# Performance work log

Hardware: AMD Instinct MI355X
Metric: run time of the kernel (lower is better)

## Reference

```python
import jax, jax.numpy as jnp
import numpy as np

B, N, CIN, COUT = 4, 4096, 64, 64

def setup_inputs() -> dict:
    key = jax.random.key(0)
    k1, k2, k3, k4, k5 = jax.random.split(key, 5)
    X = jax.random.normal(k1, (B, N, CIN), dtype=jnp.float32)
    A = jax.random.uniform(k2, (N, N), dtype=jnp.float32)
    weight1 = jax.random.normal(k3, (CIN, COUT), dtype=jnp.float32) * 0.05
    weight2 = jax.random.normal(k4, (1 * COUT, COUT), dtype=jnp.float32) * 0.05
    alpha = jax.random.normal(k5, (2 * COUT, 1), dtype=jnp.float32) * 0.05
    return {"X": X, "A": A, "weight1": weight1, "weight2": weight2, "alpha": alpha}

def reference(X, A, weight1, weight2, alpha):
    n = A.shape[0]
    c = weight1.shape[1]
    b = X.shape[0]
    # add self loops on the adjacency diagonal
    idx = jnp.arange(n)
    adj = A.at[idx, idx].set(1.0)
    # node transform: [B,N,C]
    out = jnp.matmul(X, weight1)
    # edge feature (P=1): [N,N,1], row-normalized over j (axis=1)
    E = adj[:, :, None]
    E_wave = E / E.sum(axis=1, keepdims=True)
    # attention scores via rank-1 decomposition of alpha
    att_l = jnp.matmul(out, alpha[:c])   # [B,N,1]
    att_r = jnp.matmul(out, alpha[c:])   # [B,N,1]
    scores = jax.nn.leaky_relu(att_l @ jnp.swapaxes(att_r, 1, 2))  # [B,N,N]
    # exp + edge-feature weighting: [P,B,N,N]
    att = jnp.einsum('bij,ijp->pbij', jnp.exp(scores), E_wave)
    # manual softmax-style normalization over neighbors j
    att = att / att.sum(axis=-1, keepdims=True)
    # aggregate: [B,N,P,C] -> [B,N,P*C]
    agg = jnp.einsum('pbij,bjc->bipc', att, out).reshape(b, n, -1)
    return jnp.matmul(agg, weight2)
```

## Files before the change

### kernel.cpp

```cpp
#include <hip/hip_runtime.h>
#include <hip/hip_bf16.h>

typedef __attribute__((ext_vector_type(8))) short short8;
typedef __attribute__((ext_vector_type(4))) float floatx4;
typedef unsigned int u32;

#define NN 4096

static __device__ __forceinline__ unsigned f2bf_rne(float x) {
    union { float f; unsigned u; } v; v.f = x;
    unsigned r = v.u + 0x7fffu + ((v.u >> 16) & 1u);
    return r >> 16;
}
static __device__ __forceinline__ float bf2f(unsigned hi) {
    union { unsigned u; float f; } v; v.u = hi << 16; return v.f;
}

__global__ __launch_bounds__(256, 4)
void prep_kernel(const float* __restrict__ X,
                 const float* __restrict__ W1,
                 const float* __restrict__ W2,
                 const float* __restrict__ alpha,
                 unsigned short* __restrict__ Gt,
                 float* __restrict__ lv,
                 float* __restrict__ rv) {
    __shared__ __align__(16) char sm[53248];
    float* W1s  = (float*)sm;
    float* W2s  = (float*)(sm + 17408);
    float* Wcst = (float*)(sm + 34816);
    float* w1s  = (float*)(sm + 52224);
    float* als  = (float*)(sm + 52736);
    float* GsT  = (float*)sm;

    const int t = threadIdx.x;
    const int row0 = blockIdx.x * 64;
    const int b = row0 >> 12, n0 = row0 & (NN - 1);
    const int w = t >> 6, lane = t & 63;
    const int m = lane & 15, q = lane >> 4;

    const int row = row0 + w * 16 + m;
    const float* xp = X + (size_t)row * 64;
    float4 x0 = *(const float4*)(xp + q * 8);
    float4 x1 = *(const float4*)(xp + q * 8 + 4);
    float4 x2 = *(const float4*)(xp + 32 + q * 8);
    float4 x3 = *(const float4*)(xp + 32 + q * 8 + 4);

    #pragma unroll
    for (int s = 0; s < 4; ++s) {
        int idx = s * 1024 + t * 4;
        int r = idx >> 6, cc = idx & 63;
        *(float4*)&W1s[r * 68 + cc] = *(const float4*)(W1 + idx);
        *(float4*)&W2s[r * 68 + cc] = *(const float4*)(W2 + idx);
    }
    if (t < 128) als[t] = alpha[t];
    __syncthreads();

    {
        const int k = t >> 2, nq = t & 3;
        float acc[16];
        #pragma unroll
        for (int i = 0; i < 16; ++i) acc[i] = 0.f;
        for (int mm = 0; mm < 64; ++mm) {
            float w1v = W1s[k * 68 + mm];
            #pragma unroll
            for (int i = 0; i < 16; ++i)
                acc[i] += w1v * W2s[mm * 68 + nq * 16 + i];
        }
        #pragma unroll
        for (int i = 0; i < 16; ++i)
            Wcst[(nq * 16 + i) * 68 + k] = acc[i];
    }
    if (t < 64) {
        float sl = 0.f, sr = 0.f;
        for (int cc2 = 0; cc2 < 64; ++cc2) {
            float wv = W1s[t * 68 + cc2];
            sl += wv * als[cc2];
            sr += wv * als[64 + cc2];
        }
        w1s[t] = sl; w1s[64 + t] = sr;
    }
    __syncthreads();

    const float xs[16] = {x0.x,x0.y,x0.z,x0.w, x1.x,x1.y,x1.z,x1.w,
                          x2.x,x2.y,x2.z,x2.w, x3.x,x3.y,x3.z,x3.w};

    float pl = 0.f, pr = 0.f;
    #pragma unroll
    for (int ks = 0; ks < 2; ++ks)
        #pragma unroll
        for (int j = 0; j < 8; ++j) {
            int k = ks * 32 + q * 8 + j;
            float xv = xs[ks * 8 + j];
            pl += xv * w1s[k];
            pr += xv * w1s[64 + k];
        }
    pl += __shfl_xor(pl, 16, 64); pl += __shfl_xor(pl, 32, 64);
    pr += __shfl_xor(pr, 16, 64); pr += __shfl_xor(pr, 32, 64);
    if (q == 0) { lv[row] = pl; rv[row] = pr; }

    short8 ah[2], al[2];
    #pragma unroll
    for (int ks = 0; ks < 2; ++ks)
        #pragma unroll
        for (int j = 0; j < 8; ++j) {
            float f = xs[ks * 8 + j];
            unsigned hb = f2bf_rne(f);
            float res = f - bf2f(hb);
            ah[ks][j] = (short)hb;
            al[ks][j] = (short)f2bf_rne(res);
        }

    short8 bfr[4][2];
    #pragma unroll
    for (int nt = 0; nt < 4; ++nt)
        #pragma unroll
        for (int ks = 0; ks < 2; ++ks) {
            const float* wp = &Wcst[(nt * 16 + m) * 68 + ks * 32 + q * 8];
            float4 w0 = *(const float4*)wp;
            float4 w1 = *(const float4*)(wp + 4);
            short8 bf;
            bf[0] = (short)f2bf_rne(w0.x); bf[1] = (short)f2bf_rne(w0.y);
            bf[2] = (short)f2bf_rne(w0.z); bf[3] = (short)f2bf_rne(w0.w);
            bf[4] = (short)f2bf_rne(w1.x); bf[5] = (short)f2bf_rne(w1.y);
            bf[6] = (short)f2bf_rne(w1.z); bf[7] = (short)f2bf_rne(w1.w);
            bfr[nt][ks] = bf;
        }

    floatx4 acc[4] = {{0,0,0,0},{0,0,0,0},{0,0,0,0},{0,0,0,0}};
    #pragma unroll
    for (int ks = 0; ks < 2; ++ks)
        #pragma unroll
        for (int nt = 0; nt < 4; ++nt) {
            acc[nt] = __builtin_amdgcn_mfma_f32_16x16x32_bf16(ah[ks], bfr[nt][ks], acc[nt], 0, 0, 0);
            acc[nt] = __builtin_amdgcn_mfma_f32_16x16x32_bf16(al[ks], bfr[nt][ks], acc[nt], 0, 0, 0);
        }

    __syncthreads();
    #pragma unroll
    for (int nt = 0; nt < 4; ++nt)
        #pragma unroll
        for (int rg = 0; rg < 4; ++rg)
            GsT[(nt * 16 + m) * 68 + w * 16 + q * 4 + rg] = acc[nt][rg];
    __syncthreads();
    unsigned* Gu = (unsigned*)Gt;
    #pragma unroll
    for (int it2 = 0; it2 < 8; ++it2) {
        int c2 = (t >> 5) + it2 * 8;
        int np = t & 31;
        unsigned lo = f2bf_rne(GsT[c2 * 68 + 2 * np]);
        unsigned hi = f2bf_rne(GsT[c2 * 68 + 2 * np + 1]);
        Gu[(((((size_t)(b * 64 + c2)) << 12) + n0) >> 1) + np] = lo | (hi << 16);
    }
}

__global__ __launch_bounds__(1024, 4)
void attn_kernel(const float* __restrict__ A,
                 const unsigned short* __restrict__ Gt,
                 const float* __restrict__ lv,
                 const float* __restrict__ rv,
                 float* __restrict__ out) {
    __shared__ __align__(16) char sm[61440];
    unsigned short* Gs = (unsigned short*)sm;

    const int bx = blockIdx.x;
    const int i0 = (bx & 63) * 64;
    const int b  = bx >> 6;
    const int t = threadIdx.x;
    const int wave = t >> 6, lane = t & 63;
    const int grp = wave >> 2, wsub = wave & 3;
    const int m = lane & 15, q = lane >> 4;
    const int irE = wsub * 16 + m;
    const int irS = wsub * 16 + (lane >> 2);
    const int jseg = lane & 3;

    const float* aRow = A + (size_t)(i0 + irE) * NN + grp * 1024 + q * 8;
    const float* rvp  = rv + (size_t)b * NN + grp * 1024 + q * 8;
    const unsigned short* gRow = Gt + (((size_t)(b * 64 + irS)) << 12) + grp * 1024 + jseg * 8;

    const float li = lv[b * NN + i0 + irE] * 1.44269504f;
    const float li001 = li * 0.01f;
    const bool diag_grp = ((i0 >> 10) == grp);
    const int jd = (i0 + irE) - grp * 1024;

    const int soff = irS * 40 + jseg * 8;
    unsigned short* GsG = Gs + grp * 2560;

    short8 sg = *(const short8*)(gRow);
    float4 a0E = *(const float4*)(aRow);
    float4 a1E = *(const float4*)(aRow + 4);
    float4 r0E = *(const float4*)(rvp);
    float4 r1E = *(const float4*)(rvp + 4);
    float4 a0O = *(const float4*)(aRow + 32);
    float4 a1O = *(const float4*)(aRow + 36);
    float4 r0O = *(const float4*)(rvp + 32);
    float4 r1O = *(const float4*)(rvp + 36);
    *(short8*)&GsG[soff] = sg;
    sg = *(const short8*)(gRow + 32);
    asm volatile("s_waitcnt lgkmcnt(0)" ::: "memory");
    __builtin_amdgcn_s_barrier();
    __builtin_amdgcn_sched_barrier(0);

    floatx4 acc0 = {0,0,0,0}, acc1 = {0,0,0,0}, acc2 = {0,0,0,0}, acc3 = {0,0,0,0};
    float dsum = 0.f;

    auto genE = [&](float4 a0, float4 a1, float4 r0, float4 r1, int chunk) -> short8 {
        float aa[8] = {a0.x, a0.y, a0.z, a0.w, a1.x, a1.y, a1.z, a1.w};
        if (diag_grp && ((jd >> 5) == chunk)) {
            const int dd = jd - (chunk * 32 + q * 8);
            #pragma unroll
            for (int e = 0; e < 8; ++e) if (dd == e) aa[e] = 1.0f;
        }
        const float rr[8] = {r0.x, r0.y, r0.z, r0.w, r1.x, r1.y, r1.z, r1.w};
        unsigned up[8];
        #pragma unroll
        for (int e = 0; e < 8; ++e) {
            float s = fmaxf(li * rr[e], li001 * rr[e]);
            float ev = __builtin_amdgcn_exp2f(s) * aa[e];
            unsigned u = __float_as_uint(ev) + 0x8000u;
            up[e] = u;
            dsum += __uint_as_float(u & 0xffff0000u);
        }
        union { unsigned u[4]; short8 s8; } cv;
        cv.u[0] = __builtin_amdgcn_perm(up[1], up[0], 0x07060302u);
        cv.u[1] = __builtin_amdgcn_perm(up[3], up[2], 0x07060302u);
        cv.u[2] = __builtin_amdgcn_perm(up[5], up[4], 0x07060302u);
        cv.u[3] = __builtin_amdgcn_perm(up[7], up[6], 0x07060302u);
        return cv.s8;
    };

    for (int cc = 0; cc < 32; cc += 2) {
        {
            *(short8*)&GsG[((cc + 1) % 3) * 10240 + soff] = sg;
            { const int jn = (cc + 2 < 32) ? (cc + 2) * 32 : 0;
              sg = *(const short8*)(gRow + jn); }
            const short8 afr = genE(a0E, a1E, r0E, r1E, cc);
            { const int jn = (cc + 2 < 32) ? (cc + 2) * 32 : 0;
              a0E = *(const float4*)(aRow + jn);
              a1E = *(const float4*)(aRow + jn + 4);
              r0E = *(const float4*)(rvp + jn);
              r1E = *(const float4*)(rvp + jn + 4); }
            const unsigned short* rb = &GsG[(cc % 3) * 10240];
            const short8 b0 = *(const short8*)&rb[( m) * 40 + q * 8];
            const short8 b1 = *(const short8*)&rb[(16 + m) * 40 + q * 8];
            const short8 b2 = *(const short8*)&rb[(32 + m) * 40 + q * 8];
            const short8 b3 = *(const short8*)&rb[(48 + m) * 40 + q * 8];
            acc0 = __builtin_amdgcn_mfma_f32_16x16x32_bf16(afr, b0, acc0, 0, 0, 0);
            acc1 = __builtin_amdgcn_mfma_f32_16x16x32_bf16(afr, b1, acc1, 0, 0, 0);
            acc2 = __builtin_amdgcn_mfma_f32_16x16x32_bf16(afr, b2, acc2, 0, 0, 0);
            acc3 = __builtin_amdgcn_mfma_f32_16x16x32_bf16(afr, b3, acc3, 0, 0, 0);
            asm volatile("s_waitcnt lgkmcnt(0)" ::: "memory");
            __builtin_amdgcn_s_barrier();
            __builtin_amdgcn_sched_barrier(0);
        }
        {
            *(short8*)&GsG[((cc + 2) % 3) * 10240 + soff] = sg;
            { const int jn = (cc + 3 < 32) ? (cc + 3) * 32 : 0;
              sg = *(const short8*)(gRow + jn); }
            const short8 afr = genE(a0O, a1O, r0O, r1O, cc + 1);
            { const int jn = (cc + 3 < 32) ? (cc + 3) * 32 : 0;
              a0O = *(const float4*)(aRow + jn);
              a1O = *(const float4*)(aRow + jn + 4);
              r0O = *(const float4*)(rvp + jn);
              r1O = *(const float4*)(rvp + jn + 4); }
            const unsigned short* rb = &GsG[((cc + 1) % 3) * 10240];
            const short8 b0 = *(const short8*)&rb[( m) * 40 + q * 8];
            const short8 b1 = *(const short8*)&rb[(16 + m) * 40 + q * 8];
            const short8 b2 = *(const short8*)&rb[(32 + m) * 40 + q * 8];
            const short8 b3 = *(const short8*)&rb[(48 + m) * 40 + q * 8];
            acc0 = __builtin_amdgcn_mfma_f32_16x16x32_bf16(afr, b0, acc0, 0, 0, 0);
            acc1 = __builtin_amdgcn_mfma_f32_16x16x32_bf16(afr, b1, acc1, 0, 0, 0);
            acc2 = __builtin_amdgcn_mfma_f32_16x16x32_bf16(afr, b2, acc2, 0, 0, 0);
            acc3 = __builtin_amdgcn_mfma_f32_16x16x32_bf16(afr, b3, acc3, 0, 0, 0);
            asm volatile("s_waitcnt lgkmcnt(0)" ::: "memory");
            __builtin_amdgcn_s_barrier();
            __builtin_amdgcn_sched_barrier(0);
        }
    }

    dsum += __shfl_xor(dsum, 16, 64);
    dsum += __shfl_xor(dsum, 32, 64);

    __syncthreads();
    float* red = (float*)sm;
    const int il = t >> 4, c4 = t & 15;
    float4 osum = {0.f, 0.f, 0.f, 0.f};
    float dtot = 0.f;
    #pragma unroll
    for (int pass = 0; pass < 2; ++pass) {
        if ((grp >> 1) == pass) {
            float* rp_ = red + (grp & 1) * 4352;
            #pragma unroll
            for (int nt = 0; nt < 4; ++nt) {
                floatx4 av = nt == 0 ? acc0 : nt == 1 ? acc1 : nt == 2 ? acc2 : acc3;
                #pragma unroll
                for (int rg = 0; rg < 4; ++rg)
                    rp_[(wsub * 16 + q * 4 + rg) * 68 + nt * 16 + m] = av[rg];
            }
            if (q == 0) rp_[(wsub * 16 + m) * 68 + 64] = dsum;
        }
        __syncthreads();
        {
            float4 v0 = *(const float4*)&red[il * 68 + c4 * 4];
            float4 v1 = *(const float4*)&red[4352 + il * 68 + c4 * 4];
            osum.x += v0.x + v1.x; osum.y += v0.y + v1.y;
            osum.z += v0.z + v1.z; osum.w += v0.w + v1.w;
            dtot += red[il * 68 + 64] + red[4352 + il * 68 + 64];
        }
        __syncthreads();
    }
    const float rinv = 1.0f / dtot;
    float4 o;
    o.x = osum.x * rinv; o.y = osum.y * rinv;
    o.z = osum.z * rinv; o.w = osum.w * rinv;
    *(float4*)(out + (((size_t)(b * NN + i0 + il)) << 6) + c4 * 4) = o;
}

extern "C" void kernel_launch(void* const* d_in, const int* in_sizes, int n_in,
                              void* d_out, int out_size, void* d_ws, size_t ws_size,
                              hipStream_t stream) {
    const float* X     = (const float*)d_in[0];
    const float* A     = (const float*)d_in[1];
    const float* W1    = (const float*)d_in[2];
    const float* W2    = (const float*)d_in[3];
    const float* alpha = (const float*)d_in[4];
    float* out = (float*)d_out;

    char* ws = (char*)d_ws;
    unsigned short* Gt = (unsigned short*)(ws);
    float* lvp = (float*)(ws + 2097152);
    float* rvp = (float*)(ws + 2097152 + 65536);

    prep_kernel<<<256, 256, 0, stream>>>(X, W1, W2, alpha, Gt, lvp, rvp);
    attn_kernel<<<256, 1024, 0, stream>>>(A, Gt, lvp, rvp, out);
}
```

Measured before the change: 157.1 us.

## Split attention over j-halves into 512 blocks with separate reduce kernel

Doubles the attention grid by splitting the neighbor (j) dimension into two halves per block, so each block processes 512 columns per group instead of 1024. Partial sums and denominators go to a workspace buffer and a new reduce kernel combines them and normalizes. It also raises MFMA priority with s_setprio around the matrix ops and adds unroll pragmas in the prep kernel. The aim is better CU occupancy on a 256-CU part, at the cost of an extra launch and partial-result traffic. Batch-interleaved block order also lets blocks sharing the same A rows run close together.

```diff
diff --git a/kernel.cpp b/kernel.cpp
--- a/kernel.cpp
+++ b/kernel.cpp
@@ -60,6 +60,7 @@
         float acc[16];
         #pragma unroll
         for (int i = 0; i < 16; ++i) acc[i] = 0.f;
+        #pragma unroll 4
         for (int mm = 0; mm < 64; ++mm) {
             float w1v = W1s[k * 68 + mm];
             #pragma unroll
@@ -72,6 +73,7 @@
     }
     if (t < 64) {
         float sl = 0.f, sr = 0.f;
+        #pragma unroll 4
         for (int cc2 = 0; cc2 < 64; ++cc2) {
             float wv = W1s[t * 68 + cc2];
             sl += wv * als[cc2];
@@ -153,18 +155,20 @@
     }
 }
 
-__global__ __launch_bounds__(1024, 4)
-void attn_kernel(const float* __restrict__ A,
-                 const unsigned short* __restrict__ Gt,
-                 const float* __restrict__ lv,
-                 const float* __restrict__ rv,
-                 float* __restrict__ out) {
+__global__ __launch_bounds__(1024, 8)
+void attn_main(const float* __restrict__ A,
+               const unsigned short* __restrict__ Gt,
+               const float* __restrict__ lv,
+               const float* __restrict__ rv,
+               float* __restrict__ pout) {
     __shared__ __align__(16) char sm[61440];
     unsigned short* Gs = (unsigned short*)sm;
 
     const int bx = blockIdx.x;
-    const int i0 = (bx & 63) * 64;
-    const int b  = bx >> 6;
+    const int b  = bx & 3;
+    const int jh = (bx >> 2) & 1;
+    const int it = bx >> 3;
+    const int i0 = it * 64;
     const int t = threadIdx.x;
     const int wave = t >> 6, lane = t & 63;
     const int grp = wave >> 2, wsub = wave & 3;
@@ -173,14 +177,17 @@
     const int irS = wsub * 16 + (lane >> 2);
     const int jseg = lane & 3;
 
-    const float* aRow = A + (size_t)(i0 + irE) * NN + grp * 1024 + q * 8;
-    const float* rvp  = rv + (size_t)b * NN + grp * 1024 + q * 8;
-    const unsigned short* gRow = Gt + (((size_t)(b * 64 + irS)) << 12) + grp * 1024 + jseg * 8;
+    const int gidx  = jh * 4 + grp;
+    const int jbase = gidx * 512;
+
+    const float* aRow = A + (size_t)(i0 + irE) * NN + jbase + q * 8;
+    const float* rvp  = rv + (size_t)b * NN + jbase + q * 8;
+    const unsigned short* gRow = Gt + (((size_t)(b * 64 + irS)) << 12) + jbase + jseg * 8;
 
     const float li = lv[b * NN + i0 + irE] * 1.44269504f;
     const float li001 = li * 0.01f;
-    const bool diag_grp = ((i0 >> 10) == grp);
-    const int jd = (i0 + irE) - grp * 1024;
+    const bool diag_grp = ((i0 >> 9) == gidx);
+    const int jd = (i0 + irE) - jbase;
 
     const int soff = irS * 40 + jseg * 8;
     unsigned short* GsG = Gs + grp * 2560;
@@ -228,13 +235,13 @@
         return cv.s8;
     };
 
-    for (int cc = 0; cc < 32; cc += 2) {
+    for (int cc = 0; cc < 16; cc += 2) {
         {
             *(short8*)&GsG[((cc + 1) % 3) * 10240 + soff] = sg;
-            { const int jn = (cc + 2 < 32) ? (cc + 2) * 32 : 0;
+            { const int jn = (cc + 2 < 16) ? (cc + 2) * 32 : 0;
               sg = *(const short8*)(gRow + jn); }
             const short8 afr = genE(a0E, a1E, r0E, r1E, cc);
-            { const int jn = (cc + 2 < 32) ? (cc + 2) * 32 : 0;
+            { const int jn = (cc + 2 < 16) ? (cc + 2) * 32 : 0;
               a0E = *(const float4*)(aRow + jn);
               a1E = *(const float4*)(aRow + jn + 4);
               r0E = *(const float4*)(rvp + jn);
@@ -244,20 +251,22 @@
             const short8 b1 = *(const short8*)&rb[(16 + m) * 40 + q * 8];
             const short8 b2 = *(const short8*)&rb[(32 + m) * 40 + q * 8];
             const short8 b3 = *(const short8*)&rb[(48 + m) * 40 + q * 8];
+            __builtin_amdgcn_s_setprio(1);
             acc0 = __builtin_amdgcn_mfma_f32_16x16x32_bf16(afr, b0, acc0, 0, 0, 0);
             acc1 = __builtin_amdgcn_mfma_f32_16x16x32_bf16(afr, b1, acc1, 0, 0, 0);
             acc2 = __builtin_amdgcn_mfma_f32_16x16x32_bf16(afr, b2, acc2, 0, 0, 0);
             acc3 = __builtin_amdgcn_mfma_f32_16x16x32_bf16(afr, b3, acc3, 0, 0, 0);
+            __builtin_amdgcn_s_setprio(0);
             asm volatile("s_waitcnt lgkmcnt(0)" ::: "memory");
             __builtin_amdgcn_s_barrier();
             __builtin_amdgcn_sched_barrier(0);
         }
         {
             *(short8*)&GsG[((cc + 2) % 3) * 10240 + soff] = sg;
-            { const int jn = (cc + 3 < 32) ? (cc + 3) * 32 : 0;
+            { const int jn = (cc + 3 < 16) ? (cc + 3) * 32 : 0;
               sg = *(const short8*)(gRow + jn); }
             const short8 afr = genE(a0O, a1O, r0O, r1O, cc + 1);
-            { const int jn = (cc + 3 < 32) ? (cc + 3) * 32 : 0;
+            { const int jn = (cc + 3 < 16) ? (cc + 3) * 32 : 0;
               a0O = *(const float4*)(aRow + jn);
               a1O = *(const float4*)(aRow + jn + 4);
               r0O = *(const float4*)(rvp + jn);
@@ -267,10 +276,12 @@
             const short8 b1 = *(const short8*)&rb[(16 + m) * 40 + q * 8];
             const short8 b2 = *(const short8*)&rb[(32 + m) * 40 + q * 8];
             const short8 b3 = *(const short8*)&rb[(48 + m) * 40 + q * 8];
+            __builtin_amdgcn_s_setprio(1);
             acc0 = __builtin_amdgcn_mfma_f32_16x16x32_bf16(afr, b0, acc0, 0, 0, 0);
             acc1 = __builtin_amdgcn_mfma_f32_16x16x32_bf16(afr, b1, acc1, 0, 0, 0);
             acc2 = __builtin_amdgcn_mfma_f32_16x16x32_bf16(afr, b2, acc2, 0, 0, 0);
             acc3 = __builtin_amdgcn_mfma_f32_16x16x32_bf16(afr, b3, acc3, 0, 0, 0);
+            __builtin_amdgcn_s_setprio(0);
             asm volatile("s_waitcnt lgkmcnt(0)" ::: "memory");
             __builtin_amdgcn_s_barrier();
             __builtin_amdgcn_sched_barrier(0);
@@ -308,11 +319,37 @@
         }
         __syncthreads();
     }
-    const float rinv = 1.0f / dtot;
-    float4 o;
-    o.x = osum.x * rinv; o.y = osum.y * rinv;
-    o.z = osum.z * rinv; o.w = osum.w * rinv;
-    *(float4*)(out + (((size_t)(b * NN + i0 + il)) << 6) + c4 * 4) = o;
+    float* pb = pout + (size_t)bx * 4352;
+    *(float4*)&pb[il * 68 + c4 * 4] = osum;
+    if (c4 == 0) pb[il * 68 + 64] = dtot;
+}
+
+__global__ __launch_bounds__(256, 4)
+void attn_reduce(const float* __restrict__ pout,
+                 float* __restrict__ out) {
+    const int bx = blockIdx.x;
+    const int it = bx & 63, b = bx >> 6;
+    const int t = threadIdx.x;
+    const int row = t >> 2, quad = t & 3;
+
+    const float* base0 = pout + (size_t)((it << 3) | (0 << 2) | b) * 4352 + row * 68;
+    const float* base1 = pout + (size_t)((it << 3) | (1 << 2) | b) * 4352 + row * 68;
+
+    float den = base0[64] + base1[64];
+    const float rinv = 1.0f / den;
+
+    float* op = out + (((size_t)(b * NN + it * 64 + row)) << 6) + quad * 16;
+    #pragma unroll
+    for (int f = 0; f < 4; ++f) {
+        const float4 v0 = *(const float4*)&base0[quad * 16 + f * 4];
+        const float4 v1 = *(const float4*)&base1[quad * 16 + f * 4];
+        float4 o;
+        o.x = (v0.x + v1.x) * rinv;
+        o.y = (v0.y + v1.y) * rinv;
+        o.z = (v0.z + v1.z) * rinv;
+        o.w = (v0.w + v1.w) * rinv;
+        *(float4*)(op + f * 4) = o;
+    }
 }
 
 extern "C" void kernel_launch(void* const* d_in, const int* in_sizes, int n_in,
@@ -327,9 +364,11 @@
 
     char* ws = (char*)d_ws;
     unsigned short* Gt = (unsigned short*)(ws);
-    float* lvp = (float*)(ws + 2097152);
-    float* rvp = (float*)(ws + 2097152 + 65536);
+    float* lvp  = (float*)(ws + 2097152);
+    float* rvp  = (float*)(ws + 2097152 + 65536);
+    float* pout = (float*)(ws + 2097152 + 131072);
 
     prep_kernel<<<256, 256, 0, stream>>>(X, W1, W2, alpha, Gt, lvp, rvp);
-    attn_kernel<<<256, 1024, 0, stream>>>(A, Gt, lvp, rvp, out);
-}
+    attn_main<<<512, 1024, 0, stream>>>(A, Gt, lvp, rvp, pout);
+    attn_reduce<<<256, 256, 0, stream>>>(pout, out);
+}
```

Measured after the change: 315.7 us. 2.01x slower.
